# Kernel optimization log

Measured on AMD Instinct MI355X. Metric: run time of the kernel, lower is better.

The kernel has to match this reference:

```python
import jax, jax.numpy as jnp
import numpy as np


def setup_inputs() -> dict:
    key = jax.random.key(0)
    k1, k2, k3, k4 = jax.random.split(key, 4)
    B, S, D = 16, 1024, 300      # batch, set_size, word_vector_dim
    K = 64                        # hidden_set_size == compressed_dim (element_dim)
    O = 256                       # set_representation_dim (output_dim)
    Xs = jax.random.normal(k1, (B, S, D), dtype=jnp.float32)
    # Linear(word_vector_dim -> hidden_set_size)
    W = jax.random.normal(k2, (K, D), dtype=jnp.float32) * (1.0 / np.sqrt(D))
    b = jax.random.normal(k3, (K,), dtype=jnp.float32) * 0.01
    # hidden_sets: (output_dim, hidden_set_size, element_dim) with xavier-normal scale
    xav = np.sqrt(2.0 / (K + K))
    hidden_sets = jax.random.normal(k4, (O, K, K), dtype=jnp.float32) * xav
    return {"Xs": Xs, "W": W, "b": b, "hidden_sets": hidden_sets}


def reference(Xs, W, b, hidden_sets):
    # compress: [B,S,D] @ [D,K] + b -> [B,S,K]
    Xc = jnp.einsum('bsd,kd->bsk', Xs, W) + b
    # bipartite_match: tensordot over element_dim -> [B,S,O,N] (N = hidden_set_size)
    G = jax.nn.relu(jnp.einsum('bsk,onk->bson', Xc, hidden_sets))
    # set_size (1024) > hidden_set_size (64): max over hidden-set axis, sum over set axis
    value = jnp.sum(jnp.max(G, axis=-1), axis=1)  # [B,O]
    return value
```

## Files before the change

kernel.cpp:

```cpp
#include <hip/hip_runtime.h>
#include <hip/hip_bf16.h>

#define B_  16
#define S_  1024
#define D_  300
#define K_  64
#define O_  256
#define M_  (B_*S_)

typedef __attribute__((ext_vector_type(8)))  short s8b;
typedef __attribute__((ext_vector_type(4)))  float f32x4;
typedef __attribute__((ext_vector_type(16))) float f32x16;

#define MFMA16(a,b,c) __builtin_amdgcn_mfma_f32_16x16x32_bf16((a),(b),(c),0,0,0)
#define MFMA32(a,b,c) __builtin_amdgcn_mfma_f32_32x32x16_bf16((a),(b),(c),0,0,0)

__device__ __forceinline__ unsigned short bf16_bits(float f) {
    return __builtin_bit_cast(unsigned short, __float2bfloat16(f));
}


#define C_BLK 512
#define H_BLK 512
#define LT    72

__global__ __launch_bounds__(256) void k_prep(
        const float* __restrict__ Xs, const float* __restrict__ W,
        const float* __restrict__ bias, const float* __restrict__ H,
        __hip_bfloat16* __restrict__ XcF, __hip_bfloat16* __restrict__ HbF) {
    __shared__ __hip_bfloat16 lt[32 * LT];
    int bx = blockIdx.x, tid = threadIdx.x;

    if (bx >= C_BLK) {
        int g8 = (bx - C_BLK) * 256 + tid;
        const float* src = H + (size_t)g8 * 8;
        float4 f0 = *(const float4*)(src);
        float4 f1 = *(const float4*)(src + 4);
        union { unsigned short us[8]; uint4 q; } pk;
        pk.us[0]=bf16_bits(f0.x); pk.us[1]=bf16_bits(f0.y);
        pk.us[2]=bf16_bits(f0.z); pk.us[3]=bf16_bits(f0.w);
        pk.us[4]=bf16_bits(f1.x); pk.us[5]=bf16_bits(f1.y);
        pk.us[6]=bf16_bits(f1.z); pk.us[7]=bf16_bits(f1.w);
        int k8 = g8 & 7, n = (g8 >> 3) & 63, o = g8 >> 9;
        int idx = o * 512 + (n >> 5) * 256 + (k8 >> 1) * 64
                + (k8 & 1) * 32 + (n & 31);
        ((uint4*)HbF)[idx] = pk.q;
        return;
    }

    int w    = tid >> 6, lane = tid & 63;
    int q    = lane >> 4, r = lane & 15;
    int lrow0 = (w & 1) * 16;
    int col0  = (w >> 1) * 32;
    int row0  = bx * 32 + lrow0;

    f32x4 acc0 = {0.f,0.f,0.f,0.f}, acc1 = {0.f,0.f,0.f,0.f};
    const float* arow  = Xs + (size_t)(row0 + r) * D_;
    const float* brow0 = W  + (size_t)(col0 + r) * D_;
    const float* brow1 = W  + (size_t)(col0 + 16 + r) * D_;
    const float4 z4 = {0.f,0.f,0.f,0.f};

#pragma unroll
    for (int ks = 0; ks < 10; ++ks) {
        int k0 = ks * 32 + q * 8;
        float4 a0 = (k0     < D_) ? *(const float4*)(arow  + k0)     : z4;
        float4 a1 = (k0 + 4 < D_) ? *(const float4*)(arow  + k0 + 4) : z4;
        float4 b0 = (k0     < D_) ? *(const float4*)(brow0 + k0)     : z4;
        float4 b1 = (k0 + 4 < D_) ? *(const float4*)(brow0 + k0 + 4) : z4;
        float4 c0 = (k0     < D_) ? *(const float4*)(brow1 + k0)     : z4;
        float4 c1 = (k0 + 4 < D_) ? *(const float4*)(brow1 + k0 + 4) : z4;
        union { unsigned short us[8]; s8b v; } pa, pb, pc;
        pa.us[0]=bf16_bits(a0.x); pa.us[1]=bf16_bits(a0.y);
        pa.us[2]=bf16_bits(a0.z); pa.us[3]=bf16_bits(a0.w);
        pa.us[4]=bf16_bits(a1.x); pa.us[5]=bf16_bits(a1.y);
        pa.us[6]=bf16_bits(a1.z); pa.us[7]=bf16_bits(a1.w);
        pb.us[0]=bf16_bits(b0.x); pb.us[1]=bf16_bits(b0.y);
        pb.us[2]=bf16_bits(b0.z); pb.us[3]=bf16_bits(b0.w);
        pb.us[4]=bf16_bits(b1.x); pb.us[5]=bf16_bits(b1.y);
        pb.us[6]=bf16_bits(b1.z); pb.us[7]=bf16_bits(b1.w);
        pc.us[0]=bf16_bits(c0.x); pc.us[1]=bf16_bits(c0.y);
        pc.us[2]=bf16_bits(c0.z); pc.us[3]=bf16_bits(c0.w);
        pc.us[4]=bf16_bits(c1.x); pc.us[5]=bf16_bits(c1.y);
        pc.us[6]=bf16_bits(c1.z); pc.us[7]=bf16_bits(c1.w);
        acc0 = MFMA16(pa.v, pb.v, acc0);
        acc1 = MFMA16(pa.v, pc.v, acc1);
    }
#pragma unroll
    for (int i = 0; i < 4; ++i) {
        int lr = lrow0 + q * 4 + i;
        int c0i = col0 + r;
        lt[lr * LT + c0i]      = __float2bfloat16(acc0[i] + bias[c0i]);
        lt[lr * LT + c0i + 16] = __float2bfloat16(acc1[i] + bias[c0i + 16]);
    }
    __syncthreads();
    {
        int l31 = tid & 31, hf = (tid >> 5) & 1, ks = tid >> 6;
        uint4 ch = *(const uint4*)(&lt[l31 * LT + ks * 16 + hf * 8]);
        ((uint4*)XcF)[bx * 256 + tid] = ch;
    }
}

__global__ __launch_bounds__(256, 4) void k_fused(
        const __hip_bfloat16* __restrict__ XcF,
        const __hip_bfloat16* __restrict__ HbF,
        float* __restrict__ out) {
    int tid   = threadIdx.x;
    int w     = tid >> 6, lane = tid & 63;
    int bx    = blockIdx.x;
    int batch = bx >> 6;
    int oq    = bx & 63;
    int o     = oq * 4 + w;

    const uint4* hb = (const uint4*)HbF;
    const uint4* xf = (const uint4*)XcF + (size_t)batch * 32 * 256;

    s8b af[2][4];
#pragma unroll
    for (int nt = 0; nt < 2; ++nt)
#pragma unroll
        for (int ks = 0; ks < 4; ++ks)
            af[nt][ks] = __builtin_bit_cast(s8b,
                hb[o * 512 + nt * 256 + ks * 64 + lane]);

    float total = 0.0f;
#pragma unroll 4
    for (int mt = 0; mt < 32; ++mt) {
        s8b bf[4];
#pragma unroll
        for (int ks = 0; ks < 4; ++ks)
            bf[ks] = __builtin_bit_cast(s8b, xf[mt * 256 + ks * 64 + lane]);

        f32x16 zz = {0.f,0.f,0.f,0.f,0.f,0.f,0.f,0.f,
                     0.f,0.f,0.f,0.f,0.f,0.f,0.f,0.f};
        f32x16 a0 = zz, a1 = zz;
#pragma unroll
        for (int ks = 0; ks < 4; ++ks) {
            a0 = MFMA32(af[0][ks], bf[ks], a0);
            a1 = MFMA32(af[1][ks], bf[ks], a1);
        }
        float p0 = fmaxf(fmaxf(a0[0],  a0[1]),  fmaxf(a0[2],  a0[3]));
        float p1 = fmaxf(fmaxf(a0[4],  a0[5]),  fmaxf(a0[6],  a0[7]));
        float p2 = fmaxf(fmaxf(a0[8],  a0[9]),  fmaxf(a0[10], a0[11]));
        float p3 = fmaxf(fmaxf(a0[12], a0[13]), fmaxf(a0[14], a0[15]));
        float q0 = fmaxf(fmaxf(a1[0],  a1[1]),  fmaxf(a1[2],  a1[3]));
        float q1 = fmaxf(fmaxf(a1[4],  a1[5]),  fmaxf(a1[6],  a1[7]));
        float q2 = fmaxf(fmaxf(a1[8],  a1[9]),  fmaxf(a1[10], a1[11]));
        float q3 = fmaxf(fmaxf(a1[12], a1[13]), fmaxf(a1[14], a1[15]));
        float v  = fmaxf(fmaxf(fmaxf(p0, p1), fmaxf(p2, p3)),
                         fmaxf(fmaxf(q0, q1), fmaxf(q2, q3)));
        v = fmaxf(v, __shfl_xor(v, 32));
        v = fmaxf(v, 0.0f);
        total += v;
    }
    total += __shfl_xor(total, 1);
    total += __shfl_xor(total, 2);
    total += __shfl_xor(total, 4);
    total += __shfl_xor(total, 8);
    total += __shfl_xor(total, 16);
    if (lane == 0) out[batch * O_ + o] = total;
}

extern "C" void kernel_launch(void* const* d_in, const int* in_sizes, int n_in,
                              void* d_out, int out_size, void* d_ws, size_t ws_size,
                              hipStream_t stream) {
    const float* Xs   = (const float*)d_in[0];
    const float* W    = (const float*)d_in[1];
    const float* bias = (const float*)d_in[2];
    const float* H    = (const float*)d_in[3];
    float* out = (float*)d_out;

    char* ws = (char*)d_ws;
    __hip_bfloat16* HbF = (__hip_bfloat16*)(ws);
    __hip_bfloat16* XcF = (__hip_bfloat16*)(ws + 2097152);

    k_prep <<<C_BLK + H_BLK, 256, 0, stream>>>(Xs, W, bias, H, XcF, HbF);
    k_fused<<<B_ * (O_ / 4), 256, 0, stream>>>(XcF, HbF, out);
}
```

Measured before the change: 113.4 us.

## Compute two hidden sets per wave, split set axis, reduce with atomics

Each wave now handles two output channels, so every loaded XcF fragment feeds four MFMAs instead of two. The set dimension is split into two halves across blocks, and partial sums are combined with atomicAdd into an output that an extra block in the prep kernel zeroes first. Block indices are remapped so that blocks sharing a batch sit close together for L2 reuse. The extra hidden-set fragments raise register use, so occupancy is lowered to 3 waves, and float atomics make the summation order nondeterministic.

New measurement: 114.5 us. Within noise of the previous version (+0.9%).

```diff
diff --git a/kernel.cpp b/kernel.cpp
--- a/kernel.cpp
+++ b/kernel.cpp
@@ -27,11 +27,19 @@
 __global__ __launch_bounds__(256) void k_prep(
         const float* __restrict__ Xs, const float* __restrict__ W,
         const float* __restrict__ bias, const float* __restrict__ H,
-        __hip_bfloat16* __restrict__ XcF, __hip_bfloat16* __restrict__ HbF) {
+        __hip_bfloat16* __restrict__ XcF, __hip_bfloat16* __restrict__ HbF,
+        float* __restrict__ out) {
     __shared__ __hip_bfloat16 lt[32 * LT];
     int bx = blockIdx.x, tid = threadIdx.x;
 
     if (bx >= C_BLK) {
+        if (bx >= C_BLK + H_BLK) {
+            float4 z = {0.f,0.f,0.f,0.f};
+            float4* o4 = (float4*)out;
+#pragma unroll
+            for (int i = 0; i < 4; ++i) o4[tid * 4 + i] = z;
+            return;
+        }
         int g8 = (bx - C_BLK) * 256 + tid;
         const float* src = H + (size_t)g8 * 8;
         float4 f0 = *(const float4*)(src);
@@ -100,31 +108,35 @@
     }
 }
 
-__global__ __launch_bounds__(256, 4) void k_fused(
+__global__ __launch_bounds__(256, 3) void k_fused(
         const __hip_bfloat16* __restrict__ XcF,
         const __hip_bfloat16* __restrict__ HbF,
         float* __restrict__ out) {
     int tid   = threadIdx.x;
     int w     = tid >> 6, lane = tid & 63;
     int bx    = blockIdx.x;
-    int batch = bx >> 6;
-    int oq    = bx & 63;
-    int o     = oq * 4 + w;
+    int batch = (bx & 7) * 2 + ((bx >> 3) & 1);
+    int og    = (bx >> 4) & 31;
+    int sh    = (bx >> 9) & 1;
+    int o0    = og * 8 + w * 2;
 
     const uint4* hb = (const uint4*)HbF;
-    const uint4* xf = (const uint4*)XcF + (size_t)batch * 32 * 256;
-
-    s8b af[2][4];
-#pragma unroll
-    for (int nt = 0; nt < 2; ++nt)
-#pragma unroll
-        for (int ks = 0; ks < 4; ++ks)
-            af[nt][ks] = __builtin_bit_cast(s8b,
-                hb[o * 512 + nt * 256 + ks * 64 + lane]);
-
-    float total = 0.0f;
-#pragma unroll 4
-    for (int mt = 0; mt < 32; ++mt) {
+    const uint4* xf = (const uint4*)XcF
+                    + (size_t)batch * (32 * 256) + (size_t)sh * (16 * 256);
+
+    s8b af[2][2][4];
+#pragma unroll
+    for (int oi = 0; oi < 2; ++oi)
+#pragma unroll
+        for (int nt = 0; nt < 2; ++nt)
+#pragma unroll
+            for (int ks = 0; ks < 4; ++ks)
+                af[oi][nt][ks] = __builtin_bit_cast(s8b,
+                    hb[(o0 + oi) * 512 + nt * 256 + ks * 64 + lane]);
+
+    float total0 = 0.0f, total1 = 0.0f;
+#pragma unroll 2
+    for (int mt = 0; mt < 16; ++mt) {
         s8b bf[4];
 #pragma unroll
         for (int ks = 0; ks < 4; ++ks)
@@ -132,32 +144,50 @@
 
         f32x16 zz = {0.f,0.f,0.f,0.f,0.f,0.f,0.f,0.f,
                      0.f,0.f,0.f,0.f,0.f,0.f,0.f,0.f};
-        f32x16 a0 = zz, a1 = zz;
+        f32x16 a00 = zz, a01 = zz, a10 = zz, a11 = zz;
 #pragma unroll
         for (int ks = 0; ks < 4; ++ks) {
-            a0 = MFMA32(af[0][ks], bf[ks], a0);
-            a1 = MFMA32(af[1][ks], bf[ks], a1);
+            a00 = MFMA32(af[0][0][ks], bf[ks], a00);
+            a01 = MFMA32(af[0][1][ks], bf[ks], a01);
+            a10 = MFMA32(af[1][0][ks], bf[ks], a10);
+            a11 = MFMA32(af[1][1][ks], bf[ks], a11);
         }
-        float p0 = fmaxf(fmaxf(a0[0],  a0[1]),  fmaxf(a0[2],  a0[3]));
-        float p1 = fmaxf(fmaxf(a0[4],  a0[5]),  fmaxf(a0[6],  a0[7]));
-        float p2 = fmaxf(fmaxf(a0[8],  a0[9]),  fmaxf(a0[10], a0[11]));
-        float p3 = fmaxf(fmaxf(a0[12], a0[13]), fmaxf(a0[14], a0[15]));
-        float q0 = fmaxf(fmaxf(a1[0],  a1[1]),  fmaxf(a1[2],  a1[3]));
-        float q1 = fmaxf(fmaxf(a1[4],  a1[5]),  fmaxf(a1[6],  a1[7]));
-        float q2 = fmaxf(fmaxf(a1[8],  a1[9]),  fmaxf(a1[10], a1[11]));
-        float q3 = fmaxf(fmaxf(a1[12], a1[13]), fmaxf(a1[14], a1[15]));
-        float v  = fmaxf(fmaxf(fmaxf(p0, p1), fmaxf(p2, p3)),
-                         fmaxf(fmaxf(q0, q1), fmaxf(q2, q3)));
-        v = fmaxf(v, __shfl_xor(v, 32));
-        v = fmaxf(v, 0.0f);
-        total += v;
-    }
-    total += __shfl_xor(total, 1);
-    total += __shfl_xor(total, 2);
-    total += __shfl_xor(total, 4);
-    total += __shfl_xor(total, 8);
-    total += __shfl_xor(total, 16);
-    if (lane == 0) out[batch * O_ + o] = total;
+        float p0 = fmaxf(fmaxf(a00[0],  a00[1]),  fmaxf(a00[2],  a00[3]));
+        float p1 = fmaxf(fmaxf(a00[4],  a00[5]),  fmaxf(a00[6],  a00[7]));
+        float p2 = fmaxf(fmaxf(a00[8],  a00[9]),  fmaxf(a00[10], a00[11]));
+        float p3 = fmaxf(fmaxf(a00[12], a00[13]), fmaxf(a00[14], a00[15]));
+        float p4 = fmaxf(fmaxf(a01[0],  a01[1]),  fmaxf(a01[2],  a01[3]));
+        float p5 = fmaxf(fmaxf(a01[4],  a01[5]),  fmaxf(a01[6],  a01[7]));
+        float p6 = fmaxf(fmaxf(a01[8],  a01[9]),  fmaxf(a01[10], a01[11]));
+        float p7 = fmaxf(fmaxf(a01[12], a01[13]), fmaxf(a01[14], a01[15]));
+        float v0 = fmaxf(fmaxf(fmaxf(p0, p1), fmaxf(p2, p3)),
+                         fmaxf(fmaxf(p4, p5), fmaxf(p6, p7)));
+        float q0 = fmaxf(fmaxf(a10[0],  a10[1]),  fmaxf(a10[2],  a10[3]));
+        float q1 = fmaxf(fmaxf(a10[4],  a10[5]),  fmaxf(a10[6],  a10[7]));
+        float q2 = fmaxf(fmaxf(a10[8],  a10[9]),  fmaxf(a10[10], a10[11]));
+        float q3 = fmaxf(fmaxf(a10[12], a10[13]), fmaxf(a10[14], a10[15]));
+        float q4 = fmaxf(fmaxf(a11[0],  a11[1]),  fmaxf(a11[2],  a11[3]));
+        float q5 = fmaxf(fmaxf(a11[4],  a11[5]),  fmaxf(a11[6],  a11[7]));
+        float q6 = fmaxf(fmaxf(a11[8],  a11[9]),  fmaxf(a11[10], a11[11]));
+        float q7 = fmaxf(fmaxf(a11[12], a11[13]), fmaxf(a11[14], a11[15]));
+        float v1 = fmaxf(fmaxf(fmaxf(q0, q1), fmaxf(q2, q3)),
+                         fmaxf(fmaxf(q4, q5), fmaxf(q6, q7)));
+        float s0 = __shfl_xor(v0, 32);
+        float s1 = __shfl_xor(v1, 32);
+        total0 += fmaxf(fmaxf(v0, s0), 0.0f);
+        total1 += fmaxf(fmaxf(v1, s1), 0.0f);
+    }
+#pragma unroll
+    for (int d = 1; d <= 16; d <<= 1) {
+        float s0 = __shfl_xor(total0, d);
+        float s1 = __shfl_xor(total1, d);
+        total0 += s0;
+        total1 += s1;
+    }
+    if (lane == 0) {
+        atomicAdd(out + batch * O_ + o0,     total0);
+        atomicAdd(out + batch * O_ + o0 + 1, total1);
+    }
 }
 
 extern "C" void kernel_launch(void* const* d_in, const int* in_sizes, int n_in,
@@ -173,6 +203,6 @@
     __hip_bfloat16* HbF = (__hip_bfloat16*)(ws);
     __hip_bfloat16* XcF = (__hip_bfloat16*)(ws + 2097152);
 
-    k_prep <<<C_BLK + H_BLK, 256, 0, stream>>>(Xs, W, bias, H, XcF, HbF);
-    k_fused<<<B_ * (O_ / 4), 256, 0, stream>>>(XcF, HbF, out);
-}
+    k_prep <<<C_BLK + H_BLK + 1, 256, 0, stream>>>(Xs, W, bias, H, XcF, HbF, out);
+    k_fused<<<1024, 256, 0, stream>>>(XcF, HbF, out);
+}
```
